# Performance work log

Measured on AMD Instinct MI355X. Metric: run time of the kernel, lower is better.

Reference implementation:

```python
import jax, jax.numpy as jnp
import numpy as np

TOP_K = 8
NUM_EXPERTS = 64


def setup_inputs() -> dict:
    key = jax.random.key(0)
    k1, k2 = jax.random.split(key)
    x = jax.random.normal(k1, (4, 4096, 2048), dtype=jnp.float32)
    # nn.Linear weight [num_experts, d_model], scaled like typical init
    gate_w = jax.random.normal(k2, (NUM_EXPERTS, 2048), dtype=jnp.float32) * 0.02
    expert_bias = jnp.zeros((NUM_EXPERTS,), dtype=jnp.float32)
    return {"x": x, "gate_w": gate_w, "expert_bias": expert_bias}


def reference(x, gate_w, expert_bias):
    # logits = gate(x): [b, s, E]
    logits = jnp.einsum("bsd,ed->bse", x, gate_w)
    # bias is detached in the original (routing-only, no grad)
    logits_with_bias = logits + jax.lax.stop_gradient(expert_bias)
    # top-k over experts
    top_k_logits, top_k_indices = jax.lax.top_k(logits_with_bias, TOP_K)
    # softmax over the small top-k dimension
    top_k_scores = jax.nn.softmax(top_k_logits, axis=-1)
    # scatter-add load counts per expert (training branch)
    flat_indices = top_k_indices.reshape(-1)
    expert_counts = jnp.zeros((NUM_EXPERTS,), dtype=jnp.int32).at[flat_indices].add(1)
    return top_k_scores, top_k_indices, expert_counts
```

## Files before the change

### kernel.cpp

```cpp
#include <hip/hip_runtime.h>
#include <math.h>

#define DIM   2048
#define NEXP  64
#define TOPK  8
#define BM    32
#define NT    512
#define NBLK  512
#define RSTRIDE 260
#define BUF1  (32 * RSTRIDE)

typedef __attribute__((ext_vector_type(8)))  short bf16x8;
typedef __attribute__((ext_vector_type(16))) float f32x16;

#define MFMA(A, B, C) __builtin_amdgcn_mfma_f32_32x32x16_bf16(A, B, C, 0, 0, 0)
#define AS_BF(v) (*(const bf16x8*)&(v))

typedef __attribute__((address_space(3))) unsigned int       lds_uint;
typedef __attribute__((address_space(1))) const unsigned int glb_uint;

#define STR2(x) #x
#define STR(x) STR2(x)
#define GL16(dst, p, off) \
    asm volatile("global_load_dwordx4 %0, %1, off offset:" STR(off) \
                 : "=v"(dst) : "v"(p) : "memory")

__device__ inline unsigned int bfpack(float a, float b) {
    unsigned int ua = __float_as_uint(a), ub = __float_as_uint(b);
    unsigned int lo = (ua + 0x7FFFu + ((ua >> 16) & 1u)) >> 16;
    unsigned int hi = (ub + 0x7FFFu + ((ub >> 16) & 1u)) & 0xFFFF0000u;
    return hi | lo;
}
__device__ inline void split2pair(float a, float b, unsigned int& h, unsigned int& m) {
    h = bfpack(a, b);
    float ra = a - __uint_as_float(h << 16);
    float rb = b - __uint_as_float(h & 0xFFFF0000u);
    m = bfpack(ra, rb);
}

__global__ __launch_bounds__(256) void prep_kernel(const float* __restrict__ w,
                                                   unsigned int* __restrict__ wpack) {
    const int u = blockIdx.x * 256 + threadIdx.x;
    const int e = u >> 8, k8 = u & 255;
    const float4 v0 = *(const float4*)(w + (size_t)e * DIM + k8 * 8);
    const float4 v1 = *(const float4*)(w + (size_t)e * DIM + k8 * 8 + 4);
    unsigned int h[4], m[4];
    split2pair(v0.x, v0.y, h[0], m[0]);
    split2pair(v0.z, v0.w, h[1], m[1]);
    split2pair(v1.x, v1.y, h[2], m[2]);
    split2pair(v1.z, v1.w, h[3], m[3]);
    const int wv = k8 >> 5, t = (k8 >> 1) & 15, kh = k8 & 1;
    const int eh = e >> 5, le = e & 31;
    char* base = (char*)wpack + (size_t)wv * 65536 + t * 4096
               + (eh * 2) * 1024 + (kh * 32 + le) * 16;
    *(uint4*)(base)        = (uint4){h[0], h[1], h[2], h[3]};
    *(uint4*)(base + 1024) = (uint4){m[0], m[1], m[2], m[3]};
}

__global__ __launch_bounds__(NT, 4) void router_kernel(
    const float* __restrict__ x,
    const unsigned int* __restrict__ wpack,
    const float* __restrict__ bias,
    float* __restrict__ out,
    int* __restrict__ histws,
    int M)
{
    __shared__ __align__(16) char smem[67584 + 256];
    float* smemf = (float*)smem;
    int* hist = (int*)(smem + 67584);

    const int tid  = threadIdx.x;
    const int bid  = blockIdx.x;
    const int swz  = (bid & 7) * (NBLK / 8) + (bid >> 3);
    const int row0 = swz * BM;
    if (tid < NEXP) hist[tid] = 0;

    const int wv   = tid >> 6;
    const int lane = tid & 63;
    const int lr   = lane & 31;
    const int kh   = lane >> 5;

    const int xr0 = 4 * wv;
    const float* xsrc0 = x + (size_t)(row0 + xr0 + 0) * DIM + lane * 4;
    const float* xsrc1 = x + (size_t)(row0 + xr0 + 1) * DIM + lane * 4;
    const float* xsrc2 = x + (size_t)(row0 + xr0 + 2) * DIM + lane * 4;
    const float* xsrc3 = x + (size_t)(row0 + xr0 + 3) * DIM + lane * 4;
    const int xo0 = (xr0 + 0) * RSTRIDE, xo1 = (xr0 + 1) * RSTRIDE,
              xo2 = (xr0 + 2) * RSTRIDE, xo3 = (xr0 + 3) * RSTRIDE;

    const char* wbase = (const char*)wpack + (2 * wv) * 4096 + lane * 16;

    const int g00 = 8 * wv + 2 * kh;
    const int a00 = lr * RSTRIDE + g00 * 4;
    const int a10 = a00 + 16;

    f32x16 acc0 = {}, acc1 = {};
    uint4 w0h_A, w0m_A, w0H_A, w0M_A, w1h_A, w1m_A, w1H_A, w1M_A;
    uint4 w0h_B, w0m_B, w0H_B, w0M_B, w1h_B, w1m_B, w1H_B, w1M_B;

#define DMA4(BUFO, PH) do { \
        __builtin_amdgcn_global_load_lds((glb_uint*)(const void*)(xsrc0 + (PH) * 256), \
                                         (lds_uint*)(void*)(smemf + (BUFO) + xo0), 16, 0, 0); \
        __builtin_amdgcn_global_load_lds((glb_uint*)(const void*)(xsrc1 + (PH) * 256), \
                                         (lds_uint*)(void*)(smemf + (BUFO) + xo1), 16, 0, 0); \
        __builtin_amdgcn_global_load_lds((glb_uint*)(const void*)(xsrc2 + (PH) * 256), \
                                         (lds_uint*)(void*)(smemf + (BUFO) + xo2), 16, 0, 0); \
        __builtin_amdgcn_global_load_lds((glb_uint*)(const void*)(xsrc3 + (PH) * 256), \
                                         (lds_uint*)(void*)(smemf + (BUFO) + xo3), 16, 0, 0); \
        asm volatile("" ::: "memory"); \
    } while (0)

#define WLD(S, PH) do { \
        const char* a_ = wbase + (PH) * 65536; \
        const char* b_ = a_ + 4096; \
        GL16(w0h_##S, a_, 0);    GL16(w0m_##S, a_, 1024); \
        GL16(w0H_##S, a_, 2048); GL16(w0M_##S, a_, 3072); \
        GL16(w1h_##S, b_, 0);    GL16(w1m_##S, b_, 1024); \
        GL16(w1H_##S, b_, 2048); GL16(w1M_##S, b_, 3072); \
    } while (0)

#define DOSPLIT(vlo, vhi, hv, mv) do { \
        unsigned int h_[4], m_[4]; \
        split2pair((vlo).x, (vlo).y, h_[0], m_[0]); \
        split2pair((vlo).z, (vlo).w, h_[1], m_[1]); \
        split2pair((vhi).x, (vhi).y, h_[2], m_[2]); \
        split2pair((vhi).z, (vhi).w, h_[3], m_[3]); \
        hv = (uint4){h_[0], h_[1], h_[2], h_[3]}; \
        mv = (uint4){m_[0], m_[1], m_[2], m_[3]}; \
    } while (0)

#define COMPUTE(S, BUFO) do { \
        float4 alo0_ = *(const float4*)(smemf + (BUFO) + a00); \
        float4 ahi0_ = *(const float4*)(smemf + (BUFO) + a00 + 4); \
        float4 alo1_ = *(const float4*)(smemf + (BUFO) + a10); \
        float4 ahi1_ = *(const float4*)(smemf + (BUFO) + a10 + 4); \
        uint4 ah_, am_; \
        DOSPLIT(alo0_, ahi0_, ah_, am_); \
        acc0 = MFMA(AS_BF(ah_), AS_BF(w0h_##S), acc0); \
        acc0 = MFMA(AS_BF(am_), AS_BF(w0h_##S), acc0); \
        acc0 = MFMA(AS_BF(ah_), AS_BF(w0m_##S), acc0); \
        acc1 = MFMA(AS_BF(ah_), AS_BF(w0H_##S), acc1); \
        acc1 = MFMA(AS_BF(am_), AS_BF(w0H_##S), acc1); \
        acc1 = MFMA(AS_BF(ah_), AS_BF(w0M_##S), acc1); \
        DOSPLIT(alo1_, ahi1_, ah_, am_); \
        acc0 = MFMA(AS_BF(ah_), AS_BF(w1h_##S), acc0); \
        acc0 = MFMA(AS_BF(am_), AS_BF(w1h_##S), acc0); \
        acc0 = MFMA(AS_BF(ah_), AS_BF(w1m_##S), acc0); \
        acc1 = MFMA(AS_BF(ah_), AS_BF(w1H_##S), acc1); \
        acc1 = MFMA(AS_BF(am_), AS_BF(w1H_##S), acc1); \
        acc1 = MFMA(AS_BF(ah_), AS_BF(w1M_##S), acc1); \
    } while (0)

#define VMW(N) do { asm volatile("s_waitcnt vmcnt(" STR(N) ")" ::: "memory"); \
                    __builtin_amdgcn_sched_barrier(0); } while (0)
#define BAR __builtin_amdgcn_s_barrier()

    DMA4(0, 0); WLD(A, 0);
    VMW(8); BAR;
    DMA4(BUF1, 1); WLD(B, 1); VMW(12); COMPUTE(A, 0);    VMW(8); BAR;
    DMA4(0,    2); WLD(A, 2); VMW(12); COMPUTE(B, BUF1); VMW(8); BAR;
    DMA4(BUF1, 3); WLD(B, 3); VMW(12); COMPUTE(A, 0);    VMW(8); BAR;
    DMA4(0,    4); WLD(A, 4); VMW(12); COMPUTE(B, BUF1); VMW(8); BAR;
    DMA4(BUF1, 5); WLD(B, 5); VMW(12); COMPUTE(A, 0);    VMW(8); BAR;
    DMA4(0,    6); WLD(A, 6); VMW(12); COMPUTE(B, BUF1); VMW(8); BAR;
    DMA4(BUF1, 7); WLD(B, 7); VMW(12); COMPUTE(A, 0);    VMW(8); BAR;
    VMW(0); COMPUTE(B, BUF1);

#undef VMW
#undef COMPUTE
#undef DOSPLIT
#undef WLD
#undef DMA4

    __syncthreads();

    float* lgf = smemf;
    #pragma unroll
    for (int r = 0; r < 16; ++r) {
        const int rr = (r & 3) + 8 * (r >> 2) + 4 * kh;
        lgf[(wv * 32 + rr) * 66 + lr]      = acc0[r];
        lgf[(wv * 32 + rr) * 66 + 32 + lr] = acc1[r];
    }
    __syncthreads();

    float* out_scores = out;
    float* out_idx    = out + (size_t)M * TOPK;

    #pragma unroll
    for (int i = 0; i < 4; ++i) {
        const int row = wv * 4 + i;
        float vm = bias[lane];
        #pragma unroll
        for (int p = 0; p < 8; ++p) vm += lgf[(p * 32 + row) * 66 + lane];

        float vals[TOPK];
        int   ids[TOPK];
        #pragma unroll
        for (int k = 0; k < TOPK; ++k) {
            float mv = vm;
            int   mi = lane;
            #pragma unroll
            for (int off = 32; off > 0; off >>= 1) {
                float ov = __shfl_xor(mv, off);
                int   oi = __shfl_xor(mi, off);
                if (ov > mv || (ov == mv && oi < mi)) { mv = ov; mi = oi; }
            }
            vals[k] = mv; ids[k] = mi;
            if (lane == mi) { vm = -INFINITY; atomicAdd(&hist[mi], 1); }
        }
        if (lane == 0) {
            const float m = vals[0];
            float e[TOPK];
            float ssum = 0.f;
            #pragma unroll
            for (int k = 0; k < TOPK; ++k) { e[k] = expf(vals[k] - m); ssum += e[k]; }
            const float inv = 1.0f / ssum;
            const size_t base = (size_t)(row0 + row) * TOPK;
            #pragma unroll
            for (int k = 0; k < TOPK; ++k) {
                out_scores[base + k] = e[k] * inv;
                out_idx[base + k]    = (float)ids[k];
            }
        }
    }

    __syncthreads();
    if (tid < NEXP) histws[bid * NEXP + tid] = hist[tid];
}

__global__ __launch_bounds__(512) void reduce_kernel(const int* __restrict__ histws,
                                                     float* __restrict__ counts) {
    __shared__ int partl[8][NEXP];
    const int t = threadIdx.x;
    const int e = t & 63, c = t >> 6;
    int sm = 0;
    for (int b = c; b < NBLK; b += 8) sm += histws[b * NEXP + e];
    partl[c][e] = sm;
    __syncthreads();
    if (t < NEXP) {
        int tot = 0;
        #pragma unroll
        for (int i = 0; i < 8; ++i) tot += partl[i][t];
        counts[t] = (float)tot;
    }
}

extern "C" void kernel_launch(void* const* d_in, const int* in_sizes, int n_in,
                              void* d_out, int out_size, void* d_ws, size_t ws_size,
                              hipStream_t stream) {
    const float* x    = (const float*)d_in[0];
    const float* w    = (const float*)d_in[1];
    const float* bias = (const float*)d_in[2];
    float* out = (float*)d_out;
    const int M = in_sizes[0] / DIM;

    unsigned int* wpack = (unsigned int*)d_ws;
    int* histws = (int*)((char*)d_ws + (1u << 20));
    float* out_counts = out + (size_t)2 * M * TOPK;

    prep_kernel<<<64, 256, 0, stream>>>(w, wpack);
    router_kernel<<<NBLK, NT, 0, stream>>>(x, wpack, bias, out, histws, M);
    reduce_kernel<<<1, 512, 0, stream>>>(histws, out_counts);
}
```

Measured before the change: 74.65 us.

## Stage x tiles through registers and single-buffer weight fragments

Replaces the direct global-to-LDS DMA loads of the x tile with ordinary 16-byte global loads into registers, followed by explicit LDS stores and an lgkmcnt wait before each barrier. The weight fragments are no longer double-buffered in two register sets. Each phase now issues the next weight load only after the MFMA block finishes, which cuts register use but leaves the weight-load latency exposed instead of overlapped with compute. The extra register round-trip for x adds VGPR traffic and LDS write instructions.

```diff
diff --git a/kernel.cpp b/kernel.cpp
--- a/kernel.cpp
+++ b/kernel.cpp
@@ -15,9 +15,6 @@
 
 #define MFMA(A, B, C) __builtin_amdgcn_mfma_f32_32x32x16_bf16(A, B, C, 0, 0, 0)
 #define AS_BF(v) (*(const bf16x8*)&(v))
-
-typedef __attribute__((address_space(3))) unsigned int       lds_uint;
-typedef __attribute__((address_space(1))) const unsigned int glb_uint;
 
 #define STR2(x) #x
 #define STR(x) STR2(x)
@@ -85,8 +82,10 @@
     const float* xsrc1 = x + (size_t)(row0 + xr0 + 1) * DIM + lane * 4;
     const float* xsrc2 = x + (size_t)(row0 + xr0 + 2) * DIM + lane * 4;
     const float* xsrc3 = x + (size_t)(row0 + xr0 + 3) * DIM + lane * 4;
-    const int xo0 = (xr0 + 0) * RSTRIDE, xo1 = (xr0 + 1) * RSTRIDE,
-              xo2 = (xr0 + 2) * RSTRIDE, xo3 = (xr0 + 3) * RSTRIDE;
+    const int xo0 = (xr0 + 0) * RSTRIDE + (lane << 2);
+    const int xo1 = (xr0 + 1) * RSTRIDE + (lane << 2);
+    const int xo2 = (xr0 + 2) * RSTRIDE + (lane << 2);
+    const int xo3 = (xr0 + 3) * RSTRIDE + (lane << 2);
 
     const char* wbase = (const char*)wpack + (2 * wv) * 4096 + lane * 16;
 
@@ -95,28 +94,30 @@
     const int a10 = a00 + 16;
 
     f32x16 acc0 = {}, acc1 = {};
-    uint4 w0h_A, w0m_A, w0H_A, w0M_A, w1h_A, w1m_A, w1H_A, w1M_A;
-    uint4 w0h_B, w0m_B, w0H_B, w0M_B, w1h_B, w1m_B, w1H_B, w1M_B;
-
-#define DMA4(BUFO, PH) do { \
-        __builtin_amdgcn_global_load_lds((glb_uint*)(const void*)(xsrc0 + (PH) * 256), \
-                                         (lds_uint*)(void*)(smemf + (BUFO) + xo0), 16, 0, 0); \
-        __builtin_amdgcn_global_load_lds((glb_uint*)(const void*)(xsrc1 + (PH) * 256), \
-                                         (lds_uint*)(void*)(smemf + (BUFO) + xo1), 16, 0, 0); \
-        __builtin_amdgcn_global_load_lds((glb_uint*)(const void*)(xsrc2 + (PH) * 256), \
-                                         (lds_uint*)(void*)(smemf + (BUFO) + xo2), 16, 0, 0); \
-        __builtin_amdgcn_global_load_lds((glb_uint*)(const void*)(xsrc3 + (PH) * 256), \
-                                         (lds_uint*)(void*)(smemf + (BUFO) + xo3), 16, 0, 0); \
-        asm volatile("" ::: "memory"); \
-    } while (0)
-
-#define WLD(S, PH) do { \
+    uint4 xr0_, xr1_, xr2_, xr3_;
+    uint4 w0h_, w0m_, w0H_, w0M_, w1h_, w1m_, w1H_, w1M_;
+
+#define XLD(PH) do { \
+        GL16(xr0_, xsrc0 + (PH) * 256, 0); \
+        GL16(xr1_, xsrc1 + (PH) * 256, 0); \
+        GL16(xr2_, xsrc2 + (PH) * 256, 0); \
+        GL16(xr3_, xsrc3 + (PH) * 256, 0); \
+    } while (0)
+
+#define WLD(PH) do { \
         const char* a_ = wbase + (PH) * 65536; \
         const char* b_ = a_ + 4096; \
-        GL16(w0h_##S, a_, 0);    GL16(w0m_##S, a_, 1024); \
-        GL16(w0H_##S, a_, 2048); GL16(w0M_##S, a_, 3072); \
-        GL16(w1h_##S, b_, 0);    GL16(w1m_##S, b_, 1024); \
-        GL16(w1H_##S, b_, 2048); GL16(w1M_##S, b_, 3072); \
+        GL16(w0h_, a_, 0);    GL16(w0m_, a_, 1024); \
+        GL16(w0H_, a_, 2048); GL16(w0M_, a_, 3072); \
+        GL16(w1h_, b_, 0);    GL16(w1m_, b_, 1024); \
+        GL16(w1H_, b_, 2048); GL16(w1M_, b_, 3072); \
+    } while (0)
+
+#define DSW(BUFO) do { \
+        *(uint4*)(smemf + (BUFO) + xo0) = xr0_; \
+        *(uint4*)(smemf + (BUFO) + xo1) = xr1_; \
+        *(uint4*)(smemf + (BUFO) + xo2) = xr2_; \
+        *(uint4*)(smemf + (BUFO) + xo3) = xr3_; \
     } while (0)
 
 #define DOSPLIT(vlo, vhi, hv, mv) do { \
@@ -129,48 +130,53 @@
         mv = (uint4){m_[0], m_[1], m_[2], m_[3]}; \
     } while (0)
 
-#define COMPUTE(S, BUFO) do { \
+#define COMPUTE(BUFO) do { \
         float4 alo0_ = *(const float4*)(smemf + (BUFO) + a00); \
         float4 ahi0_ = *(const float4*)(smemf + (BUFO) + a00 + 4); \
         float4 alo1_ = *(const float4*)(smemf + (BUFO) + a10); \
         float4 ahi1_ = *(const float4*)(smemf + (BUFO) + a10 + 4); \
         uint4 ah_, am_; \
         DOSPLIT(alo0_, ahi0_, ah_, am_); \
-        acc0 = MFMA(AS_BF(ah_), AS_BF(w0h_##S), acc0); \
-        acc0 = MFMA(AS_BF(am_), AS_BF(w0h_##S), acc0); \
-        acc0 = MFMA(AS_BF(ah_), AS_BF(w0m_##S), acc0); \
-        acc1 = MFMA(AS_BF(ah_), AS_BF(w0H_##S), acc1); \
-        acc1 = MFMA(AS_BF(am_), AS_BF(w0H_##S), acc1); \
-        acc1 = MFMA(AS_BF(ah_), AS_BF(w0M_##S), acc1); \
+        acc0 = MFMA(AS_BF(ah_), AS_BF(w0h_), acc0); \
+        acc0 = MFMA(AS_BF(am_), AS_BF(w0h_), acc0); \
+        acc0 = MFMA(AS_BF(ah_), AS_BF(w0m_), acc0); \
+        acc1 = MFMA(AS_BF(ah_), AS_BF(w0H_), acc1); \
+        acc1 = MFMA(AS_BF(am_), AS_BF(w0H_), acc1); \
+        acc1 = MFMA(AS_BF(ah_), AS_BF(w0M_), acc1); \
         DOSPLIT(alo1_, ahi1_, ah_, am_); \
-        acc0 = MFMA(AS_BF(ah_), AS_BF(w1h_##S), acc0); \
-        acc0 = MFMA(AS_BF(am_), AS_BF(w1h_##S), acc0); \
-        acc0 = MFMA(AS_BF(ah_), AS_BF(w1m_##S), acc0); \
-        acc1 = MFMA(AS_BF(ah_), AS_BF(w1H_##S), acc1); \
-        acc1 = MFMA(AS_BF(am_), AS_BF(w1H_##S), acc1); \
-        acc1 = MFMA(AS_BF(ah_), AS_BF(w1M_##S), acc1); \
+        acc0 = MFMA(AS_BF(ah_), AS_BF(w1h_), acc0); \
+        acc0 = MFMA(AS_BF(am_), AS_BF(w1h_), acc0); \
+        acc0 = MFMA(AS_BF(ah_), AS_BF(w1m_), acc0); \
+        acc1 = MFMA(AS_BF(ah_), AS_BF(w1H_), acc1); \
+        acc1 = MFMA(AS_BF(am_), AS_BF(w1H_), acc1); \
+        acc1 = MFMA(AS_BF(ah_), AS_BF(w1M_), acc1); \
     } while (0)
 
 #define VMW(N) do { asm volatile("s_waitcnt vmcnt(" STR(N) ")" ::: "memory"); \
                     __builtin_amdgcn_sched_barrier(0); } while (0)
+#define LGK0 asm volatile("s_waitcnt lgkmcnt(0)" ::: "memory")
 #define BAR __builtin_amdgcn_s_barrier()
 
-    DMA4(0, 0); WLD(A, 0);
-    VMW(8); BAR;
-    DMA4(BUF1, 1); WLD(B, 1); VMW(12); COMPUTE(A, 0);    VMW(8); BAR;
-    DMA4(0,    2); WLD(A, 2); VMW(12); COMPUTE(B, BUF1); VMW(8); BAR;
-    DMA4(BUF1, 3); WLD(B, 3); VMW(12); COMPUTE(A, 0);    VMW(8); BAR;
-    DMA4(0,    4); WLD(A, 4); VMW(12); COMPUTE(B, BUF1); VMW(8); BAR;
-    DMA4(BUF1, 5); WLD(B, 5); VMW(12); COMPUTE(A, 0);    VMW(8); BAR;
-    DMA4(0,    6); WLD(A, 6); VMW(12); COMPUTE(B, BUF1); VMW(8); BAR;
-    DMA4(BUF1, 7); WLD(B, 7); VMW(12); COMPUTE(A, 0);    VMW(8); BAR;
-    VMW(0); COMPUTE(B, BUF1);
+    XLD(0); WLD(0);
+    VMW(8);
+    DSW(0); LGK0; BAR;
+
+    XLD(1); VMW(4); COMPUTE(0);    WLD(1); VMW(8); DSW(BUF1); LGK0; BAR;
+    XLD(2); VMW(4); COMPUTE(BUF1); WLD(2); VMW(8); DSW(0);    LGK0; BAR;
+    XLD(3); VMW(4); COMPUTE(0);    WLD(3); VMW(8); DSW(BUF1); LGK0; BAR;
+    XLD(4); VMW(4); COMPUTE(BUF1); WLD(4); VMW(8); DSW(0);    LGK0; BAR;
+    XLD(5); VMW(4); COMPUTE(0);    WLD(5); VMW(8); DSW(BUF1); LGK0; BAR;
+    XLD(6); VMW(4); COMPUTE(BUF1); WLD(6); VMW(8); DSW(0);    LGK0; BAR;
+    XLD(7); VMW(4); COMPUTE(0);    WLD(7); VMW(8); DSW(BUF1); LGK0; BAR;
+    VMW(0); COMPUTE(BUF1);
 
 #undef VMW
+#undef LGK0
 #undef COMPUTE
 #undef DOSPLIT
+#undef DSW
 #undef WLD
-#undef DMA4
+#undef XLD
 
     __syncthreads();
 
```

Result: faster. 69.02 us (-7.5%).
